# Optimization experiments

Hardware: AMD Instinct MI355X
Metric: run time of the kernel (lower is better)

## Reference

```python
import jax, jax.numpy as jnp
import numpy as np

B = 4096           # batch size
NG = 4096          # num_gene_sets (columns of input)
G = 1024           # number of aggregation groups
GS = 32            # members per group (CSR-packed; code handles ragged too)
T = G * GS         # total flat indices


def setup_inputs() -> dict:
    key = jax.random.key(0)
    k1, k2, k3 = jax.random.split(key, 3)
    gene_set_features = jax.random.normal(k1, (B, NG), dtype=jnp.float32)
    att_weights = jax.random.normal(k2, (T,), dtype=jnp.float32)  # concat of per-group logits
    flat_idx = jax.random.randint(k3, (T,), 0, NG, dtype=jnp.int64)
    segment_ids = (jnp.arange(T, dtype=jnp.int64) // GS)          # sorted group id per entry
    return {
        "gene_set_features": gene_set_features,
        "att_weights": att_weights,
        "flat_idx": flat_idx,
        "segment_ids": segment_ids,
        "num_segments": G,
    }


def reference(gene_set_features, att_weights, flat_idx, segment_ids, num_segments):
    # Per-group (segment) softmax over the batch-independent attention logits.
    seg_max = jax.ops.segment_max(att_weights, segment_ids, num_segments=num_segments)
    ex = jnp.exp(att_weights - seg_max[segment_ids])
    denom = jax.ops.segment_sum(ex, segment_ids, num_segments=num_segments)
    attn = ex / denom[segment_ids]                     # (T,) softmax weights per group
    # Gather all group members for every batch row in one shot, weight, segment-sum.
    gathered = gene_set_features[:, flat_idx]          # (B, T)
    weighted = gathered * attn[None, :]                # (B, T)
    out = jax.ops.segment_sum(weighted.T, segment_ids, num_segments=num_segments).T  # (B, G)
    return out
```

## Files before the change

### kernel.cpp

```cpp
#include <hip/hip_runtime.h>

#define NGK 4096
#define BK 4096
#define GK 1024
#define GSK 32
#define TK (GK * GSK)

#define BTILE 4
#define AGG_THREADS 512

__global__ __launch_bounds__(256) void seg_softmax_kernel(
        const float* __restrict__ att,
        const int*   __restrict__ idx,
        float2*      __restrict__ pairsT) {
    int t = blockIdx.x * 256 + threadIdx.x;
    float w = att[t];

    float m = w;
    #pragma unroll
    for (int d = 16; d >= 1; d >>= 1) m = fmaxf(m, __shfl_xor(m, d, 32));
    float e = expf(w - m);
    float s = e;
    #pragma unroll
    for (int d = 16; d >= 1; d >>= 1) s += __shfl_xor(s, d, 32);

    int g = t >> 5;
    int j = t & 31;
    pairsT[j * GK + g] = make_float2(e / s, __int_as_float(idx[t]));
}

__global__ __launch_bounds__(AGG_THREADS, 4) void agg_kernel(
        const float*  __restrict__ F,
        const float2* __restrict__ pairsT,
        float*        __restrict__ out) {
    __shared__ float lds[NGK * BTILE];

    const int tid = threadIdx.x;
    const int b0 = blockIdx.x * BTILE;

    #pragma unroll
    for (int it = 0; it < NGK / AGG_THREADS; ++it) {
        int c = tid + it * AGG_THREADS;
        float4 v;
        v.x = F[(b0 + 0) * NGK + c];
        v.y = F[(b0 + 1) * NGK + c];
        v.z = F[(b0 + 2) * NGK + c];
        v.w = F[(b0 + 3) * NGK + c];
        *reinterpret_cast<float4*>(&lds[c << 2]) = v;
    }
    __syncthreads();

    #pragma unroll
    for (int k = 0; k < GK / AGG_THREADS; ++k) {
        int g = tid + k * AGG_THREADS;
        float ax = 0.f, ay = 0.f, az = 0.f, aw = 0.f;
        #pragma unroll 8
        for (int j = 0; j < GSK; ++j) {
            float2 pr = pairsT[j * GK + g];
            float w = pr.x;
            int   c = __float_as_int(pr.y);
            const float4 v = *reinterpret_cast<const float4*>(&lds[c << 2]);
            ax += w * v.x;
            ay += w * v.y;
            az += w * v.z;
            aw += w * v.w;
        }
        out[(b0 + 0) * GK + g] = ax;
        out[(b0 + 1) * GK + g] = ay;
        out[(b0 + 2) * GK + g] = az;
        out[(b0 + 3) * GK + g] = aw;
    }
}

extern "C" void kernel_launch(void* const* d_in, const int* in_sizes, int n_in,
                              void* d_out, int out_size, void* d_ws, size_t ws_size,
                              hipStream_t stream) {
    const float* F   = (const float*)d_in[0];
    const float* att = (const float*)d_in[1];
    const int*   idx = (const int*)d_in[2];

    float2* pairsT = (float2*)d_ws;
    float*  out    = (float*)d_out;

    seg_softmax_kernel<<<TK / 256, 256, 0, stream>>>(att, idx, pairsT);
    agg_kernel<<<BK / BTILE, AGG_THREADS, 0, stream>>>(F, pairsT, out);
}
```

Baseline: 119.2 us.

## Stage features in LDS as bf16 and pack two pairs per 16-byte load

After: 113.8 us. -4.6%, faster.

```diff
diff --git a/kernel.cpp b/kernel.cpp
--- a/kernel.cpp
+++ b/kernel.cpp
@@ -9,10 +9,18 @@
 #define BTILE 4
 #define AGG_THREADS 512
 
+__device__ __forceinline__ unsigned pack2bf16(float a, float b) {
+    unsigned ua = __float_as_uint(a);
+    unsigned ub = __float_as_uint(b);
+    ua = (ua + 0x7fffu + ((ua >> 16) & 1u)) >> 16;
+    ub = (ub + 0x7fffu + ((ub >> 16) & 1u)) >> 16;
+    return ua | (ub << 16);
+}
+
 __global__ __launch_bounds__(256) void seg_softmax_kernel(
         const float* __restrict__ att,
         const int*   __restrict__ idx,
-        float2*      __restrict__ pairsT) {
+        float4*      __restrict__ pairsQ) {
     int t = blockIdx.x * 256 + threadIdx.x;
     float w = att[t];
 
@@ -26,14 +34,15 @@
 
     int g = t >> 5;
     int j = t & 31;
-    pairsT[j * GK + g] = make_float2(e / s, __int_as_float(idx[t]));
+    float2 v = make_float2(e / s, __int_as_float(idx[t] << 3));
+    reinterpret_cast<float2*>(&pairsQ[(j >> 1) * GK + g])[j & 1] = v;
 }
 
-__global__ __launch_bounds__(AGG_THREADS, 4) void agg_kernel(
+__global__ __launch_bounds__(AGG_THREADS, 5) void agg_kernel(
         const float*  __restrict__ F,
-        const float2* __restrict__ pairsT,
+        const float4* __restrict__ pairsQ,
         float*        __restrict__ out) {
-    __shared__ float lds[NGK * BTILE];
+    __shared__ unsigned lds2[NGK * 2];
 
     const int tid = threadIdx.x;
     const int b0 = blockIdx.x * BTILE;
@@ -41,29 +50,42 @@
     #pragma unroll
     for (int it = 0; it < NGK / AGG_THREADS; ++it) {
         int c = tid + it * AGG_THREADS;
-        float4 v;
-        v.x = F[(b0 + 0) * NGK + c];
-        v.y = F[(b0 + 1) * NGK + c];
-        v.z = F[(b0 + 2) * NGK + c];
-        v.w = F[(b0 + 3) * NGK + c];
-        *reinterpret_cast<float4*>(&lds[c << 2]) = v;
+        float v0 = F[(b0 + 0) * NGK + c];
+        float v1 = F[(b0 + 1) * NGK + c];
+        float v2 = F[(b0 + 2) * NGK + c];
+        float v3 = F[(b0 + 3) * NGK + c];
+        uint2 q;
+        q.x = pack2bf16(v0, v1);
+        q.y = pack2bf16(v2, v3);
+        *reinterpret_cast<uint2*>(&lds2[c * 2]) = q;
     }
     __syncthreads();
+
+    const char* ldsb = reinterpret_cast<const char*>(lds2);
 
     #pragma unroll
     for (int k = 0; k < GK / AGG_THREADS; ++k) {
         int g = tid + k * AGG_THREADS;
         float ax = 0.f, ay = 0.f, az = 0.f, aw = 0.f;
-        #pragma unroll 8
-        for (int j = 0; j < GSK; ++j) {
-            float2 pr = pairsT[j * GK + g];
-            float w = pr.x;
-            int   c = __float_as_int(pr.y);
-            const float4 v = *reinterpret_cast<const float4*>(&lds[c << 2]);
-            ax += w * v.x;
-            ay += w * v.y;
-            az += w * v.z;
-            aw += w * v.w;
+        #pragma unroll 4
+        for (int jj = 0; jj < GSK / 2; ++jj) {
+            float4 pr = pairsQ[jj * GK + g];
+            {
+                uint2 q = *reinterpret_cast<const uint2*>(ldsb + __float_as_int(pr.y));
+                float w = pr.x;
+                ax += w * __uint_as_float(q.x << 16);
+                ay += w * __uint_as_float(q.x & 0xffff0000u);
+                az += w * __uint_as_float(q.y << 16);
+                aw += w * __uint_as_float(q.y & 0xffff0000u);
+            }
+            {
+                uint2 q = *reinterpret_cast<const uint2*>(ldsb + __float_as_int(pr.w));
+                float w = pr.z;
+                ax += w * __uint_as_float(q.x << 16);
+                ay += w * __uint_as_float(q.x & 0xffff0000u);
+                az += w * __uint_as_float(q.y << 16);
+                aw += w * __uint_as_float(q.y & 0xffff0000u);
+            }
         }
         out[(b0 + 0) * GK + g] = ax;
         out[(b0 + 1) * GK + g] = ay;
@@ -79,9 +101,9 @@
     const float* att = (const float*)d_in[1];
     const int*   idx = (const int*)d_in[2];
 
-    float2* pairsT = (float2*)d_ws;
+    float4* pairsQ = (float4*)d_ws;
     float*  out    = (float*)d_out;
 
-    seg_softmax_kernel<<<TK / 256, 256, 0, stream>>>(att, idx, pairsT);
-    agg_kernel<<<BK / BTILE, AGG_THREADS, 0, stream>>>(F, pairsT, out);
+    seg_softmax_kernel<<<TK / 256, 256, 0, stream>>>(att, idx, pairsQ);
+    agg_kernel<<<BK / BTILE, AGG_THREADS, 0, stream>>>(F, pairsQ, out);
 }
```
